# Kernel optimization log

Measured on AMD Instinct MI355X. Metric: run time of the kernel, lower is better.

Reference implementation:

```python
import jax, jax.numpy as jnp
import numpy as np

N_ITERATIONS = 3
N_OUT_CAPS = 10


def squash(t, axis=-2):
    # squash(s) = ||s||^2 * s / ((1 + ||s||^2) * ||s||)
    sqr_norm = jnp.sum(t * t, axis=axis, keepdims=True)
    norm = jnp.sqrt(sqr_norm)
    return sqr_norm * t / ((1.0 + sqr_norm) * norm)


def setup_inputs() -> dict:
    key = jax.random.key(0)
    B, I, O, D = 256, 1152, 10, 16
    u_hat = jax.random.normal(key, (B, I, O, D, 1), dtype=jnp.float32)
    return {"u_hat": u_hat}


def reference(u_hat):
    B = u_hat.shape[0]
    I, O = u_hat.shape[1], u_hat.shape[2]
    # routing logits b: (B, I, O, 1, 1)
    b = jnp.zeros((B, I, O, 1, 1), dtype=u_hat.dtype)
    v = None
    for r in range(N_ITERATIONS):
        c = jax.nn.softmax(b, axis=1)                 # softmax over input capsules
        s = jnp.sum(c * u_hat, axis=1, keepdims=True)  # (B, 1, O, D, 1)
        v = squash(s, axis=-2)
        if r < N_ITERATIONS - 1:
            # u_hat^T @ v: (B,I,O,1,D) @ (B,1,O,D,1) -> (B,I,O,1,1)
            b = b + jnp.matmul(jnp.swapaxes(u_hat, -2, -1), v)
    return v.reshape(B, N_OUT_CAPS, -1)
```

## Files before the change

### kernel.cpp

```cpp
#include <hip/hip_runtime.h>
#include <math.h>

#define N_I 1152
#define N_O 10
#define N_D 16
#define BLK 256
#define KPT 18

__global__ __launch_bounds__(BLK, 4)
void caps_route(const float* __restrict__ u_hat, float* __restrict__ out)
{
    __shared__ float scr_s[4][16];
    __shared__ float scr_e[4];
    __shared__ __align__(16) float vcum[16];

    const int tid  = threadIdx.x;
    const int wave = tid >> 6;
    const int lane = tid & 63;
    const int d4   = tid & 3;
    const int ig   = tid >> 2;

    const int bid = blockIdx.x;
    const int nwg = gridDim.x;
    int wid = bid;
    if ((nwg & 7) == 0) wid = (bid & 7) * (nwg >> 3) + (bid >> 3);
    const int b = wid / N_O;
    const int o = wid - b * N_O;

    const float* gbase = u_hat + (size_t)b * (N_I * N_O * N_D)
                               + (size_t)o * N_D + d4 * 4;

    float4 u[KPT];
    float4 s4 = make_float4(0.f, 0.f, 0.f, 0.f);
    #pragma unroll
    for (int k = 0; k < KPT; ++k) {
        const int i = ig + (k << 6);
        u[k] = *(const float4*)(gbase + (size_t)i * (N_O * N_D));
        s4.x += u[k].x; s4.y += u[k].y;
        s4.z += u[k].z; s4.w += u[k].w;
    }
    if (tid < 16) vcum[tid] = 0.0f;

    float4 vc = make_float4(0.f, 0.f, 0.f, 0.f);

    for (int r = 0; r < 3; ++r) {
        float esum;
        if (r == 0) {
            esum = (float)KPT;
        } else {
            s4 = make_float4(0.f, 0.f, 0.f, 0.f);
            esum = 0.0f;
            #pragma unroll
            for (int k = 0; k < KPT; ++k) {
                float p = u[k].x*vc.x + u[k].y*vc.y + u[k].z*vc.z + u[k].w*vc.w;
                p += __shfl_xor(p, 1);
                p += __shfl_xor(p, 2);
                const float e = __expf(p);
                esum += e;
                s4.x += e*u[k].x; s4.y += e*u[k].y;
                s4.z += e*u[k].z; s4.w += e*u[k].w;
            }
        }
        #pragma unroll
        for (int m = 4; m <= 32; m <<= 1) {
            s4.x += __shfl_xor(s4.x, m);
            s4.y += __shfl_xor(s4.y, m);
            s4.z += __shfl_xor(s4.z, m);
            s4.w += __shfl_xor(s4.w, m);
            esum += __shfl_xor(esum, m);
        }
        if (lane < 4) {
            scr_s[wave][lane*4+0] = s4.x;
            scr_s[wave][lane*4+1] = s4.y;
            scr_s[wave][lane*4+2] = s4.z;
            scr_s[wave][lane*4+3] = s4.w;
            if (lane == 0) scr_e[wave] = esum;
        }
        __syncthreads();
        if (tid < 16) {
            float s = 0.f, et = 0.f;
            #pragma unroll
            for (int w = 0; w < 4; ++w) { s += scr_s[w][tid]; et += scr_e[w]; }
            s /= et;
            float sq = s * s;
            sq += __shfl_xor(sq, 1);
            sq += __shfl_xor(sq, 2);
            sq += __shfl_xor(sq, 4);
            sq += __shfl_xor(sq, 8);
            const float nrm = sqrtf(sq);
            const float v = s * (nrm / (1.0f + sq));
            if (r == 2) out[(size_t)wid * N_D + tid] = v;
            else        vcum[tid] += v;
        }
        __syncthreads();
        if (r < 2) vc = ((const float4*)vcum)[d4];
    }
}

extern "C" void kernel_launch(void* const* d_in, const int* in_sizes, int n_in,
                              void* d_out, int out_size, void* d_ws, size_t ws_size,
                              hipStream_t stream)
{
    const float* u_hat = (const float*)d_in[0];
    float* out = (float*)d_out;
    const int B = in_sizes[0] / (N_I * N_O * N_D);
    hipLaunchKernelGGL(caps_route, dim3(B * N_O), dim3(BLK), 0, stream, u_hat, out);
}
```

Measured before the change: 35.06 us.

## Process five output capsules per block with double-buffered register tiles

Each block now handles five consecutive output capsules of one batch instead of one. The register tile for the next capsule is loaded while the current one is being routed, so global load latency overlaps the routing compute and barriers. This cuts the grid from 2560 to 512 blocks and doubles register pressure, with launch bounds relaxed to two blocks per SIMD. The risks are lower occupancy, possible spills, and fewer blocks to spread across CUs. The XCD-aware block remapping is also dropped.

```diff
diff --git a/kernel.cpp b/kernel.cpp
--- a/kernel.cpp
+++ b/kernel.cpp
@@ -6,8 +6,10 @@
 #define N_D 16
 #define BLK 256
 #define KPT 18
+#define NITEM 5
+#define ROWS (N_O * N_D)
 
-__global__ __launch_bounds__(BLK, 4)
+__global__ __launch_bounds__(BLK, 2)
 void caps_route(const float* __restrict__ u_hat, float* __restrict__ out)
 {
     __shared__ float scr_s[4][16];
@@ -21,80 +23,95 @@
     const int ig   = tid >> 2;
 
     const int bid = blockIdx.x;
-    const int nwg = gridDim.x;
-    int wid = bid;
-    if ((nwg & 7) == 0) wid = (bid & 7) * (nwg >> 3) + (bid >> 3);
-    const int b = wid / N_O;
-    const int o = wid - b * N_O;
+    const int b   = bid >> 1;
+    const int o0  = (bid & 1) * NITEM;
 
-    const float* gbase = u_hat + (size_t)b * (N_I * N_O * N_D)
-                               + (size_t)o * N_D + d4 * 4;
+    const float* ptr = u_hat + (size_t)b * (N_I * ROWS) + (size_t)o0 * N_D
+                     + (size_t)ig * ROWS + (size_t)d4 * 4;
+    float* outb = out + ((size_t)b * N_O + o0) * N_D;
 
-    float4 u[KPT];
-    float4 s4 = make_float4(0.f, 0.f, 0.f, 0.f);
-    #pragma unroll
-    for (int k = 0; k < KPT; ++k) {
-        const int i = ig + (k << 6);
-        u[k] = *(const float4*)(gbase + (size_t)i * (N_O * N_D));
-        s4.x += u[k].x; s4.y += u[k].y;
-        s4.z += u[k].z; s4.w += u[k].w;
-    }
-    if (tid < 16) vcum[tid] = 0.0f;
+    auto load_tile = [&](float4 (&u)[KPT], int t) {
+        const float* g = ptr + t * N_D;
+        #pragma unroll
+        for (int k = 0; k < KPT; ++k)
+            u[k] = *(const float4*)(g + (size_t)(k << 6) * ROWS);
+    };
 
-    float4 vc = make_float4(0.f, 0.f, 0.f, 0.f);
+    auto route_item = [&](const float4 (&u)[KPT], int t) {
+        if (tid < 16) vcum[tid] = 0.0f;
+        float4 vc = make_float4(0.f, 0.f, 0.f, 0.f);
+        #pragma unroll
+        for (int r = 0; r < 3; ++r) {
+            float4 s4 = make_float4(0.f, 0.f, 0.f, 0.f);
+            float esum;
+            if (r == 0) {
+                #pragma unroll
+                for (int k = 0; k < KPT; ++k) {
+                    s4.x += u[k].x; s4.y += u[k].y;
+                    s4.z += u[k].z; s4.w += u[k].w;
+                }
+                esum = (float)KPT;
+            } else {
+                esum = 0.0f;
+                #pragma unroll
+                for (int k = 0; k < KPT; ++k) {
+                    float p = u[k].x*vc.x + u[k].y*vc.y
+                            + u[k].z*vc.z + u[k].w*vc.w;
+                    p += __shfl_xor(p, 1);
+                    p += __shfl_xor(p, 2);
+                    const float e = __expf(p);
+                    esum += e;
+                    s4.x += e*u[k].x; s4.y += e*u[k].y;
+                    s4.z += e*u[k].z; s4.w += e*u[k].w;
+                }
+            }
+            #pragma unroll
+            for (int m = 4; m <= 32; m <<= 1) {
+                s4.x += __shfl_xor(s4.x, m);
+                s4.y += __shfl_xor(s4.y, m);
+                s4.z += __shfl_xor(s4.z, m);
+                s4.w += __shfl_xor(s4.w, m);
+                esum += __shfl_xor(esum, m);
+            }
+            if (lane < 4) {
+                scr_s[wave][lane*4+0] = s4.x;
+                scr_s[wave][lane*4+1] = s4.y;
+                scr_s[wave][lane*4+2] = s4.z;
+                scr_s[wave][lane*4+3] = s4.w;
+                if (lane == 0) scr_e[wave] = esum;
+            }
+            __syncthreads();
+            if (tid < 16) {
+                float s = 0.f, et = 0.f;
+                #pragma unroll
+                for (int w = 0; w < 4; ++w) { s += scr_s[w][tid]; et += scr_e[w]; }
+                s /= et;
+                float sq = s * s;
+                sq += __shfl_xor(sq, 1);
+                sq += __shfl_xor(sq, 2);
+                sq += __shfl_xor(sq, 4);
+                sq += __shfl_xor(sq, 8);
+                const float nrm = sqrtf(sq);
+                const float v = s * (nrm / (1.0f + sq));
+                if (r == 2) outb[t * N_D + tid] = v;
+                else        vcum[tid] += v;
+            }
+            __syncthreads();
+            if (r < 2) vc = ((const float4*)vcum)[d4];
+        }
+    };
 
-    for (int r = 0; r < 3; ++r) {
-        float esum;
-        if (r == 0) {
-            esum = (float)KPT;
-        } else {
-            s4 = make_float4(0.f, 0.f, 0.f, 0.f);
-            esum = 0.0f;
-            #pragma unroll
-            for (int k = 0; k < KPT; ++k) {
-                float p = u[k].x*vc.x + u[k].y*vc.y + u[k].z*vc.z + u[k].w*vc.w;
-                p += __shfl_xor(p, 1);
-                p += __shfl_xor(p, 2);
-                const float e = __expf(p);
-                esum += e;
-                s4.x += e*u[k].x; s4.y += e*u[k].y;
-                s4.z += e*u[k].z; s4.w += e*u[k].w;
-            }
-        }
-        #pragma unroll
-        for (int m = 4; m <= 32; m <<= 1) {
-            s4.x += __shfl_xor(s4.x, m);
-            s4.y += __shfl_xor(s4.y, m);
-            s4.z += __shfl_xor(s4.z, m);
-            s4.w += __shfl_xor(s4.w, m);
-            esum += __shfl_xor(esum, m);
-        }
-        if (lane < 4) {
-            scr_s[wave][lane*4+0] = s4.x;
-            scr_s[wave][lane*4+1] = s4.y;
-            scr_s[wave][lane*4+2] = s4.z;
-            scr_s[wave][lane*4+3] = s4.w;
-            if (lane == 0) scr_e[wave] = esum;
-        }
-        __syncthreads();
-        if (tid < 16) {
-            float s = 0.f, et = 0.f;
-            #pragma unroll
-            for (int w = 0; w < 4; ++w) { s += scr_s[w][tid]; et += scr_e[w]; }
-            s /= et;
-            float sq = s * s;
-            sq += __shfl_xor(sq, 1);
-            sq += __shfl_xor(sq, 2);
-            sq += __shfl_xor(sq, 4);
-            sq += __shfl_xor(sq, 8);
-            const float nrm = sqrtf(sq);
-            const float v = s * (nrm / (1.0f + sq));
-            if (r == 2) out[(size_t)wid * N_D + tid] = v;
-            else        vcum[tid] += v;
-        }
-        __syncthreads();
-        if (r < 2) vc = ((const float4*)vcum)[d4];
-    }
+    float4 uA[KPT], uB[KPT];
+    load_tile(uA, 0);
+    load_tile(uB, 1);
+    route_item(uA, 0);
+    load_tile(uA, 2);
+    route_item(uB, 1);
+    load_tile(uB, 3);
+    route_item(uA, 2);
+    load_tile(uA, 4);
+    route_item(uB, 3);
+    route_item(uA, 4);
 }
 
 extern "C" void kernel_launch(void* const* d_in, const int* in_sizes, int n_in,
@@ -104,5 +121,5 @@
     const float* u_hat = (const float*)d_in[0];
     float* out = (float*)d_out;
     const int B = in_sizes[0] / (N_I * N_O * N_D);
-    hipLaunchKernelGGL(caps_route, dim3(B * N_O), dim3(BLK), 0, stream, u_hat, out);
+    hipLaunchKernelGGL(caps_route, dim3(B * 2), dim3(BLK), 0, stream, u_hat, out);
 }
```

Result: slower. 62.15 us (+77.3%).

## Make kernel persistent over a fixed grid and prefetch next item during routing

Applied to the files above, without the earlier changes.

Replaces one-block-per-(batch,out-capsule) launch with a fixed 1024-block grid where each block processes two or three items. During the last routing iteration of an item, the next item's u_hat tile is loaded into registers so that load latency overlaps the reduction and squash. The item assignment is hardcoded for items between 2048 and 3072 and assumes the remainder divides evenly into 8 groups, so other batch sizes would be mishandled. Register pressure and reuse of the u array across items may affect occupancy.

```diff
diff --git a/kernel.cpp b/kernel.cpp
--- a/kernel.cpp
+++ b/kernel.cpp
@@ -6,49 +6,39 @@
 #define N_D 16
 #define BLK 256
 #define KPT 18
+#define ROWS (N_O * N_D)
+#define GRID 1024
 
-__global__ __launch_bounds__(BLK, 4)
-void caps_route(const float* __restrict__ u_hat, float* __restrict__ out)
+__device__ __forceinline__ const float* item_ptr(const float* u_hat, int wid,
+                                                 int ig, int d4)
 {
-    __shared__ float scr_s[4][16];
-    __shared__ float scr_e[4];
-    __shared__ __align__(16) float vcum[16];
-
-    const int tid  = threadIdx.x;
-    const int wave = tid >> 6;
-    const int lane = tid & 63;
-    const int d4   = tid & 3;
-    const int ig   = tid >> 2;
-
-    const int bid = blockIdx.x;
-    const int nwg = gridDim.x;
-    int wid = bid;
-    if ((nwg & 7) == 0) wid = (bid & 7) * (nwg >> 3) + (bid >> 3);
     const int b = wid / N_O;
     const int o = wid - b * N_O;
+    return u_hat + (size_t)b * (N_I * ROWS) + (size_t)o * N_D
+                 + (size_t)ig * ROWS + (size_t)(d4 << 2);
+}
 
-    const float* gbase = u_hat + (size_t)b * (N_I * N_O * N_D)
-                               + (size_t)o * N_D + d4 * 4;
-
-    float4 u[KPT];
-    float4 s4 = make_float4(0.f, 0.f, 0.f, 0.f);
+template<bool PRE>
+__device__ __forceinline__ void route_item(
+    float4 (&u)[KPT], const float* __restrict__ gnext,
+    float* __restrict__ outp,
+    int tid, int wave, int lane, int d4,
+    float (*scr_s)[16], float* scr_e, float* vcum)
+{
+    if (tid < 16) vcum[tid] = 0.0f;
+    float4 vc = make_float4(0.f, 0.f, 0.f, 0.f);
     #pragma unroll
-    for (int k = 0; k < KPT; ++k) {
-        const int i = ig + (k << 6);
-        u[k] = *(const float4*)(gbase + (size_t)i * (N_O * N_D));
-        s4.x += u[k].x; s4.y += u[k].y;
-        s4.z += u[k].z; s4.w += u[k].w;
-    }
-    if (tid < 16) vcum[tid] = 0.0f;
-
-    float4 vc = make_float4(0.f, 0.f, 0.f, 0.f);
-
     for (int r = 0; r < 3; ++r) {
+        float4 s4 = make_float4(0.f, 0.f, 0.f, 0.f);
         float esum;
         if (r == 0) {
+            #pragma unroll
+            for (int k = 0; k < KPT; ++k) {
+                s4.x += u[k].x; s4.y += u[k].y;
+                s4.z += u[k].z; s4.w += u[k].w;
+            }
             esum = (float)KPT;
         } else {
-            s4 = make_float4(0.f, 0.f, 0.f, 0.f);
             esum = 0.0f;
             #pragma unroll
             for (int k = 0; k < KPT; ++k) {
@@ -60,6 +50,13 @@
                 s4.x += e*u[k].x; s4.y += e*u[k].y;
                 s4.z += e*u[k].z; s4.w += e*u[k].w;
             }
+        }
+        if (PRE && r == 2) {
+            __builtin_amdgcn_sched_barrier(0);
+            #pragma unroll
+            for (int k = 0; k < KPT; ++k)
+                u[k] = *(const float4*)(gnext + (size_t)(k << 6) * ROWS);
+            __builtin_amdgcn_sched_barrier(0);
         }
         #pragma unroll
         for (int m = 4; m <= 32; m <<= 1) {
@@ -89,11 +86,59 @@
             sq += __shfl_xor(sq, 8);
             const float nrm = sqrtf(sq);
             const float v = s * (nrm / (1.0f + sq));
-            if (r == 2) out[(size_t)wid * N_D + tid] = v;
+            if (r == 2) outp[tid] = v;
             else        vcum[tid] += v;
         }
         __syncthreads();
         if (r < 2) vc = ((const float4*)vcum)[d4];
+    }
+}
+
+__global__ __launch_bounds__(BLK, 4)
+void caps_route(const float* __restrict__ u_hat, float* __restrict__ out,
+                int items)
+{
+    __shared__ float scr_s[4][16];
+    __shared__ float scr_e[4];
+    __shared__ __align__(16) float vcum[16];
+
+    const int tid  = threadIdx.x;
+    const int wave = tid >> 6;
+    const int lane = tid & 63;
+    const int d4   = tid & 3;
+    const int ig   = tid >> 2;
+
+    const int bid  = blockIdx.x;
+    const int slot = (bid & 7) * (GRID >> 3) + (bid >> 3);
+
+    const int rem    = items - 2 * GRID;
+    const int rpx    = rem >> 3;
+    const int within = slot & ((GRID >> 3) - 1);
+    const bool extra = within < rpx;
+    const int wid3   = 2 * GRID + (slot >> 7) * rpx + within;
+
+    int wid = slot;
+    const float* g0 = item_ptr(u_hat, wid, ig, d4);
+    float4 u[KPT];
+    #pragma unroll
+    for (int k = 0; k < KPT; ++k)
+        u[k] = *(const float4*)(g0 + (size_t)(k << 6) * ROWS);
+
+    route_item<true>(u, item_ptr(u_hat, slot + GRID, ig, d4),
+                     out + (size_t)wid * N_D, tid, wave, lane, d4,
+                     scr_s, scr_e, vcum);
+    wid = slot + GRID;
+    if (extra) {
+        route_item<true>(u, item_ptr(u_hat, wid3, ig, d4),
+                         out + (size_t)wid * N_D, tid, wave, lane, d4,
+                         scr_s, scr_e, vcum);
+        route_item<false>(u, (const float*)0,
+                          out + (size_t)wid3 * N_D, tid, wave, lane, d4,
+                          scr_s, scr_e, vcum);
+    } else {
+        route_item<false>(u, (const float*)0,
+                          out + (size_t)wid * N_D, tid, wave, lane, d4,
+                          scr_s, scr_e, vcum);
     }
 }
 
@@ -104,5 +149,7 @@
     const float* u_hat = (const float*)d_in[0];
     float* out = (float*)d_out;
     const int B = in_sizes[0] / (N_I * N_O * N_D);
-    hipLaunchKernelGGL(caps_route, dim3(B * N_O), dim3(BLK), 0, stream, u_hat, out);
+    const int items = B * N_O;
+    hipLaunchKernelGGL(caps_route, dim3(GRID), dim3(BLK), 0, stream,
+                       u_hat, out, items);
 }
```

After: 42.83 us. 22.2% more time.

## Process two output capsules per block for contiguous 128-byte row loads

Applied to the files above, without the earlier changes.

Each 512-thread block now handles a pair of output capsules for one batch element, with lanes arranged so each group of 8 threads reads 32 contiguous floats (128 bytes) of an input-capsule row instead of 64 bytes. This improves memory coalescing and halves the number of blocks. The reduction is adjusted to keep two separate sums per block. In exchange, block size doubles and fewer blocks fit per CU, which may reduce latency hiding.

```diff
diff --git a/kernel.cpp b/kernel.cpp
--- a/kernel.cpp
+++ b/kernel.cpp
@@ -4,42 +4,44 @@
 #define N_I 1152
 #define N_O 10
 #define N_D 16
-#define BLK 256
+#define BLK 512
 #define KPT 18
+#define ROWS (N_O * N_D)
 
-__global__ __launch_bounds__(BLK, 4)
+__global__ __launch_bounds__(BLK, 2)
 void caps_route(const float* __restrict__ u_hat, float* __restrict__ out)
 {
-    __shared__ float scr_s[4][16];
-    __shared__ float scr_e[4];
-    __shared__ __align__(16) float vcum[16];
+    __shared__ float scr_s[8][2][16];
+    __shared__ float scr_e[8][2];
+    __shared__ __align__(16) float vcum[2][16];
 
-    const int tid  = threadIdx.x;
-    const int wave = tid >> 6;
-    const int lane = tid & 63;
-    const int d4   = tid & 3;
-    const int ig   = tid >> 2;
+    const int tid   = threadIdx.x;
+    const int wave  = tid >> 6;
+    const int lane  = tid & 63;
+    const int dquad = tid & 3;
+    const int osub  = (tid >> 2) & 1;
+    const int irow  = tid >> 3;
 
     const int bid = blockIdx.x;
     const int nwg = gridDim.x;
     int wid = bid;
     if ((nwg & 7) == 0) wid = (bid & 7) * (nwg >> 3) + (bid >> 3);
-    const int b = wid / N_O;
-    const int o = wid - b * N_O;
+    const int b    = wid / 5;
+    const int pair = wid - b * 5;
 
-    const float* gbase = u_hat + (size_t)b * (N_I * N_O * N_D)
-                               + (size_t)o * N_D + d4 * 4;
+    const float* gptr = u_hat + (size_t)b * (N_I * ROWS)
+                      + (size_t)irow * ROWS
+                      + (pair << 5) + (osub << 4) + (dquad << 2);
 
     float4 u[KPT];
     float4 s4 = make_float4(0.f, 0.f, 0.f, 0.f);
     #pragma unroll
     for (int k = 0; k < KPT; ++k) {
-        const int i = ig + (k << 6);
-        u[k] = *(const float4*)(gbase + (size_t)i * (N_O * N_D));
+        u[k] = *(const float4*)(gptr + (size_t)(k << 6) * ROWS);
         s4.x += u[k].x; s4.y += u[k].y;
         s4.z += u[k].z; s4.w += u[k].w;
     }
-    if (tid < 16) vcum[tid] = 0.0f;
+    if (tid < 32) vcum[tid >> 4][tid & 15] = 0.0f;
 
     float4 vc = make_float4(0.f, 0.f, 0.f, 0.f);
 
@@ -62,25 +64,27 @@
             }
         }
         #pragma unroll
-        for (int m = 4; m <= 32; m <<= 1) {
+        for (int m = 8; m <= 32; m <<= 1) {
             s4.x += __shfl_xor(s4.x, m);
             s4.y += __shfl_xor(s4.y, m);
             s4.z += __shfl_xor(s4.z, m);
             s4.w += __shfl_xor(s4.w, m);
             esum += __shfl_xor(esum, m);
         }
-        if (lane < 4) {
-            scr_s[wave][lane*4+0] = s4.x;
-            scr_s[wave][lane*4+1] = s4.y;
-            scr_s[wave][lane*4+2] = s4.z;
-            scr_s[wave][lane*4+3] = s4.w;
-            if (lane == 0) scr_e[wave] = esum;
+        if (lane < 8) {
+            scr_s[wave][lane >> 2][(lane & 3)*4 + 0] = s4.x;
+            scr_s[wave][lane >> 2][(lane & 3)*4 + 1] = s4.y;
+            scr_s[wave][lane >> 2][(lane & 3)*4 + 2] = s4.z;
+            scr_s[wave][lane >> 2][(lane & 3)*4 + 3] = s4.w;
+            if ((lane & 3) == 0) scr_e[wave][lane >> 2] = esum;
         }
         __syncthreads();
-        if (tid < 16) {
+        if (tid < 32) {
+            const int j = tid >> 4;
+            const int d = tid & 15;
             float s = 0.f, et = 0.f;
             #pragma unroll
-            for (int w = 0; w < 4; ++w) { s += scr_s[w][tid]; et += scr_e[w]; }
+            for (int w = 0; w < 8; ++w) { s += scr_s[w][j][d]; et += scr_e[w][j]; }
             s /= et;
             float sq = s * s;
             sq += __shfl_xor(sq, 1);
@@ -89,11 +93,11 @@
             sq += __shfl_xor(sq, 8);
             const float nrm = sqrtf(sq);
             const float v = s * (nrm / (1.0f + sq));
-            if (r == 2) out[(size_t)wid * N_D + tid] = v;
-            else        vcum[tid] += v;
+            if (r == 2) out[((size_t)b * N_O + (pair << 1) + j) * N_D + d] = v;
+            else        vcum[j][d] += v;
         }
         __syncthreads();
-        if (r < 2) vc = ((const float4*)vcum)[d4];
+        if (r < 2) vc = *(const float4*)&vcum[osub][dquad << 2];
     }
 }
 
@@ -104,5 +108,5 @@
     const float* u_hat = (const float*)d_in[0];
     float* out = (float*)d_out;
     const int B = in_sizes[0] / (N_I * N_O * N_D);
-    hipLaunchKernelGGL(caps_route, dim3(B * N_O), dim3(BLK), 0, stream, u_hat, out);
+    hipLaunchKernelGGL(caps_route, dim3(B * 5), dim3(BLK), 0, stream, u_hat, out);
 }
```

Result: slower. 35.99 us (+2.7%).
